# Kernel optimization log

Hardware: AMD Instinct MI355X
Metric: run time of the kernel (lower is better)

## Reference

```python
import jax, jax.numpy as jnp
import numpy as np

MIN_NORM = 1e-15


def _dist_matrix(offset, normal, c):
    # compute_rel (default path, trip_sel='all', abs/norm/hier_trip = False):
    # dist_matrix[i, j] = exp( dist2plane(x=offset[i], a=normal_scaled[j], p=offset[j], signed=True) )
    # normal_scaled = normal * (1 - c * ||offset||^2)  (conformal factor per row)
    conf = 1.0 - c * jnp.sum(offset * offset, axis=1, keepdims=True)  # [N,1]
    a = normal * conf                                                 # [N,d]
    x2 = jnp.sum(offset * offset, axis=1)                             # [N]
    gram = offset @ offset.T                                          # [N,N], <x_i, p_j>
    # mobius_add(-p_j, x_i, c): u = -p_j, v = x_i
    uv = -gram                                                        # <u_j, v_i>, indexed [i,j]
    coef_u = 1.0 + 2.0 * c * uv + c * x2[:, None]                     # multiplies u = -p_j
    coef_v = 1.0 - c * x2[None, :]                                    # multiplies v = x_i  (||u_j||^2 = x2[j])
    denom = 1.0 + 2.0 * c * uv + (c * c) * x2[None, :] * x2[:, None]
    denom = jnp.maximum(denom, MIN_NORM)
    # diff[i,j,:]  [N,N,d]
    diff = (coef_u[:, :, None] * (-offset)[None, :, :] + coef_v[:, :, None] * offset[:, None, :]) / denom[:, :, None]
    dn2 = jnp.maximum(jnp.sum(diff * diff, axis=-1), MIN_NORM)        # [N,N]
    sc_diff_a = jnp.einsum('ijd,jd->ij', diff, a)                     # signed inner product
    a_norm = jnp.maximum(jnp.linalg.norm(a, axis=-1), MIN_NORM)       # [N]
    sqrt_c = jnp.sqrt(c)
    num = 2.0 * sqrt_c * sc_diff_a
    den = jnp.maximum((1.0 - c * dn2) * a_norm[None, :], MIN_NORM)
    dist = jnp.arcsinh(num / den) / sqrt_c
    return jnp.exp(dist)  # default branch: dist_matrix = dist_matrix.exp()


def setup_inputs() -> dict:
    key = jax.random.key(0)
    k1, k2, k3 = jax.random.split(key, 3)
    N, d = 320, 256
    # points inside the Poincare ball (||offset|| ~ 0.5 < 1 for c = 1)
    offset = jax.random.normal(k1, (N, d), jnp.float32) * 0.03
    normal = jax.random.normal(k2, (N, d), jnp.float32)
    curv = jnp.ones((1,), jnp.float32)
    # sparse triplet validity mask, as produced by get_triplet_mask
    valid_indices = jax.random.bernoulli(k3, 0.01, (N, N, N))
    return {"offset": offset, "normal": normal, "curv": curv, "valid_indices": valid_indices}


def reference(offset, normal, curv, valid_indices):
    c = curv[0]
    margin = 0.0  # __init__ value; updated only in update_distance
    dm = _dist_matrix(offset, normal, c)                 # [N,N]
    # triplet_loss = margin - d(a,p) + d(a,n), masked, clamped at 0
    tl = margin - dm[:, :, None] + dm[:, None, :]        # [N,N,N]
    tl = valid_indices.astype(dm.dtype) * tl
    tl = jnp.maximum(tl, 0.0)
    # trip_sel == 'all': mean over entries > 1e-16
    pos = tl > 1e-16
    count = jnp.maximum(jnp.sum(pos), 1)
    loss = jnp.sum(jnp.where(pos, tl, 0.0)) / count
    return loss
```

## Files before the change

kernel.cpp:

```cpp
#include <hip/hip_runtime.h>
#include <math.h>

#define NPT 320
#define DDIM 256
#define NN2 (NPT*NPT)
#define MINN 1e-15f

#define CHUNKS 5
#define PLANE4 (NN2/4)
#define CHUNK4 (PLANE4/CHUNKS)
#define ITERS  (CHUNK4/256)
#define NBLK   (NPT*CHUNKS)

__global__ __launch_bounds__(256) void k_pre(const float* __restrict__ off,
                                             const float* __restrict__ nrm,
                                             const float* __restrict__ curv,
                                             float* __restrict__ dm) {
    __shared__ float sOI[16][260];
    __shared__ float sOJ[16][260];
    __shared__ float sNJ[16][260];
    __shared__ float sx2i[16], sx2j[16], snnj[16], spaj[16];
    const float c = curv[0];
    const float sqrtc = sqrtf(c);
    const int I0 = blockIdx.y * 16, J0 = blockIdx.x * 16;
    const int t = threadIdx.x;
    const int r = t >> 4;
    const int cc = t & 15;
    const int cb = cc << 4;

    const float4* pOI = (const float4*)&off[(I0 + r) * DDIM + cb];
    const float4* pOJ = (const float4*)&off[(J0 + r) * DDIM + cb];
    const float4* pNJ = (const float4*)&nrm[(J0 + r) * DDIM + cb];
#pragma unroll
    for (int q = 0; q < 4; ++q) {
        *(float4*)&sOI[r][cb + 4 * q] = pOI[q];
        *(float4*)&sOJ[r][cb + 4 * q] = pOJ[q];
        *(float4*)&sNJ[r][cb + 4 * q] = pNJ[q];
    }
    __syncthreads();

    float a0 = 0.f, a1 = 0.f, a2 = 0.f, a3 = 0.f;
#pragma unroll
    for (int q = 0; q < 16; ++q) {
        const float oi = sOI[r][cb + q];
        const float oj = sOJ[r][cb + q];
        const float nj = sNJ[r][cb + q];
        a0 = fmaf(oi, oi, a0);
        a1 = fmaf(oj, oj, a1);
        a2 = fmaf(nj, nj, a2);
        a3 = fmaf(oj, nj, a3);
    }
    for (int o = 1; o < 16; o <<= 1) {
        a0 += __shfl_xor(a0, o);
        a1 += __shfl_xor(a1, o);
        a2 += __shfl_xor(a2, o);
        a3 += __shfl_xor(a3, o);
    }
    if (cc == 0) { sx2i[r] = a0; sx2j[r] = a1; snnj[r] = a2; spaj[r] = a3; }
    __syncthreads();

    const int ti = t >> 4, tj = t & 15;
    float g = 0.f, h = 0.f;
#pragma unroll 8
    for (int d = 0; d < DDIM; ++d) {
        const float oi = sOI[ti][d];
        g = fmaf(oi, sOJ[tj][d], g);
        h = fmaf(oi, sNJ[tj][d], h);
    }

    const float x2i = sx2i[ti], x2j = sx2j[tj], nnj = snnj[tj], paj = spaj[tj];
    const float cu = 1.f - 2.f * c * g + c * x2i;
    const float cv = 1.f - c * x2j;
    float den0 = 1.f - 2.f * c * g + c * c * x2i * x2j;
    den0 = fmaxf(den0, MINN);
    float dn2 = (cu * cu * x2j - 2.f * cu * cv * g + cv * cv * x2i) / (den0 * den0);
    dn2 = fmaxf(dn2, MINN);
    const float sc = cv * (cv * h - cu * paj) / den0;
    const float an = fmaxf(fabsf(cv) * sqrtf(nnj), MINN);
    const float numv = 2.f * sqrtc * sc;
    const float denv = fmaxf((1.f - c * dn2) * an, MINN);
    const float z = numv / denv;
    const float dist = asinhf(z) / sqrtc;
    dm[(I0 + ti) * NPT + (J0 + tj)] = expf(dist);
}

__global__ __launch_bounds__(256) void k_trip(const int* __restrict__ mask,
                                              const float* __restrict__ dm,
                                              double* __restrict__ psum,
                                              unsigned* __restrict__ pcnt) {
    __shared__ __align__(16) float dmrow[NPT];
    const int bx = blockIdx.x;
    const int i = bx / CHUNKS;
    const int chunk = bx - i * CHUNKS;
    const int t = threadIdx.x;

    for (int v = t; v < NPT; v += 256) dmrow[v] = dm[i * NPT + v];
    __syncthreads();

    const int4* m4 = (const int4*)mask + (size_t)i * PLANE4 + (size_t)chunk * CHUNK4;
    const float4* dm4 = (const float4*)dmrow;

    float s = 0.f;
    unsigned cnt = 0;

#define PROC(B, U) { \
        const unsigned lin = (unsigned)(chunk * CHUNK4 + t + 256 * (U)); \
        const unsigned jj = lin / 80u; \
        const unsigned k4 = lin - jj * 80u; \
        const float dij = dmrow[jj]; \
        const float4 dk = dm4[k4]; \
        const float t0 = dk.x - dij, t1 = dk.y - dij, t2 = dk.z - dij, t3 = dk.w - dij; \
        const bool p0 = (B).x && (t0 > 1e-16f); \
        const bool p1 = (B).y && (t1 > 1e-16f); \
        const bool p2 = (B).z && (t2 > 1e-16f); \
        const bool p3 = (B).w && (t3 > 1e-16f); \
        s += p0 ? t0 : 0.f; cnt += p0; \
        s += p1 ? t1 : 0.f; cnt += p1; \
        s += p2 ? t2 : 0.f; cnt += p2; \
        s += p3 ? t3 : 0.f; cnt += p3; }

#pragma unroll 1
    for (int g = 0; g < ITERS / 4; ++g) {
        const int u0 = g * 4;
        const int4 b0 = m4[t + 256 * (u0 + 0)];
        const int4 b1 = m4[t + 256 * (u0 + 1)];
        const int4 b2 = m4[t + 256 * (u0 + 2)];
        const int4 b3 = m4[t + 256 * (u0 + 3)];
        PROC(b0, u0 + 0)
        PROC(b1, u0 + 1)
        PROC(b2, u0 + 2)
        PROC(b3, u0 + 3)
    }
#undef PROC

    double sd = (double)s;
    for (int o = 32; o; o >>= 1) {
        sd += __shfl_down(sd, o);
        cnt += __shfl_down(cnt, o);
    }
    __shared__ double ss[4];
    __shared__ unsigned scn[4];
    const int w = t >> 6;
    if ((t & 63) == 0) { ss[w] = sd; scn[w] = cnt; }
    __syncthreads();
    if (t == 0) {
        psum[bx] = ss[0] + ss[1] + ss[2] + ss[3];
        pcnt[bx] = scn[0] + scn[1] + scn[2] + scn[3];
    }
}

__global__ __launch_bounds__(256) void k_fin(const double* __restrict__ psum,
                                             const unsigned* __restrict__ pcnt,
                                             float* __restrict__ out) {
    const int t = threadIdx.x;
    double s = 0.0;
    unsigned long long c = 0ULL;
    for (int v = t; v < NBLK; v += 256) {
        s += psum[v];
        c += (unsigned long long)pcnt[v];
    }
    for (int o = 32; o; o >>= 1) {
        s += __shfl_down(s, o);
        c += __shfl_down(c, o);
    }
    __shared__ double ss[4];
    __shared__ unsigned long long sc[4];
    const int w = t >> 6;
    if ((t & 63) == 0) { ss[w] = s; sc[w] = c; }
    __syncthreads();
    if (t == 0) {
        const double S = ss[0] + ss[1] + ss[2] + ss[3];
        unsigned long long C = sc[0] + sc[1] + sc[2] + sc[3];
        if (C == 0ULL) C = 1ULL;
        out[0] = (float)(S / (double)C);
    }
}

extern "C" void kernel_launch(void* const* d_in, const int* in_sizes, int n_in,
                              void* d_out, int out_size, void* d_ws, size_t ws_size,
                              hipStream_t stream) {
    const float* off  = (const float*)d_in[0];
    const float* nrm  = (const float*)d_in[1];
    const float* curv = (const float*)d_in[2];
    const int*   mask = (const int*)d_in[3];
    float* out = (float*)d_out;

    char* ws = (char*)d_ws;
    float* dm = (float*)(ws + 64);
    double* psum = (double*)(ws + 64 + 409600);
    unsigned* pcnt = (unsigned*)(ws + 64 + 409600 + NBLK * 8);

    k_pre<<<dim3(NPT / 16, NPT / 16), 256, 0, stream>>>(off, nrm, curv, dm);
    k_trip<<<NBLK, 256, 0, stream>>>(mask, dm, psum, pcnt);
    k_fin<<<1, 256, 0, stream>>>(psum, pcnt, out);
}
```

Before: 37.97 us.

## Read k_pre operands from global memory and reshape k_trip grid to 320 threads

k_pre no longer stages the offset and normal rows in shared memory. Each thread now streams float4 rows directly from global memory for both the norm computation and the dot products, relying on cache reuse. k_trip switches to 8 chunks per row with 320 threads per block and fully unrolled mask loads (ten int4 loads per thread) to raise memory-level parallelism. The direct global loads in k_pre risk more cache traffic, since each row is reread many times without an explicit shared-memory copy.

```diff
diff --git a/kernel.cpp b/kernel.cpp
--- a/kernel.cpp
+++ b/kernel.cpp
@@ -6,19 +6,17 @@
 #define NN2 (NPT*NPT)
 #define MINN 1e-15f
 
-#define CHUNKS 5
+#define CHUNKS 8
 #define PLANE4 (NN2/4)
 #define CHUNK4 (PLANE4/CHUNKS)
-#define ITERS  (CHUNK4/256)
+#define TTHR   320
+#define ITERS  (CHUNK4/TTHR)
 #define NBLK   (NPT*CHUNKS)
 
 __global__ __launch_bounds__(256) void k_pre(const float* __restrict__ off,
                                              const float* __restrict__ nrm,
                                              const float* __restrict__ curv,
                                              float* __restrict__ dm) {
-    __shared__ float sOI[16][260];
-    __shared__ float sOJ[16][260];
-    __shared__ float sNJ[16][260];
     __shared__ float sx2i[16], sx2j[16], snnj[16], spaj[16];
     const float c = curv[0];
     const float sqrtc = sqrtf(c);
@@ -26,46 +24,46 @@
     const int t = threadIdx.x;
     const int r = t >> 4;
     const int cc = t & 15;
-    const int cb = cc << 4;
 
-    const float4* pOI = (const float4*)&off[(I0 + r) * DDIM + cb];
-    const float4* pOJ = (const float4*)&off[(J0 + r) * DDIM + cb];
-    const float4* pNJ = (const float4*)&nrm[(J0 + r) * DDIM + cb];
+    {
+        const float4* oi = (const float4*)&off[(I0 + r) * DDIM];
+        const float4* oj = (const float4*)&off[(J0 + r) * DDIM];
+        const float4* nj = (const float4*)&nrm[(J0 + r) * DDIM];
+        float a0 = 0.f, a1 = 0.f, a2 = 0.f, a3 = 0.f;
 #pragma unroll
-    for (int q = 0; q < 4; ++q) {
-        *(float4*)&sOI[r][cb + 4 * q] = pOI[q];
-        *(float4*)&sOJ[r][cb + 4 * q] = pOJ[q];
-        *(float4*)&sNJ[r][cb + 4 * q] = pNJ[q];
+        for (int q = 0; q < 4; ++q) {
+            const float4 x = oi[cc * 4 + q];
+            const float4 y = oj[cc * 4 + q];
+            const float4 z = nj[cc * 4 + q];
+            a0 = fmaf(x.x, x.x, fmaf(x.y, x.y, fmaf(x.z, x.z, fmaf(x.w, x.w, a0))));
+            a1 = fmaf(y.x, y.x, fmaf(y.y, y.y, fmaf(y.z, y.z, fmaf(y.w, y.w, a1))));
+            a2 = fmaf(z.x, z.x, fmaf(z.y, z.y, fmaf(z.z, z.z, fmaf(z.w, z.w, a2))));
+            a3 = fmaf(y.x, z.x, fmaf(y.y, z.y, fmaf(y.z, z.z, fmaf(y.w, z.w, a3))));
+        }
+        for (int o = 1; o < 16; o <<= 1) {
+            a0 += __shfl_xor(a0, o);
+            a1 += __shfl_xor(a1, o);
+            a2 += __shfl_xor(a2, o);
+            a3 += __shfl_xor(a3, o);
+        }
+        if (cc == 0) { sx2i[r] = a0; sx2j[r] = a1; snnj[r] = a2; spaj[r] = a3; }
     }
     __syncthreads();
 
-    float a0 = 0.f, a1 = 0.f, a2 = 0.f, a3 = 0.f;
-#pragma unroll
-    for (int q = 0; q < 16; ++q) {
-        const float oi = sOI[r][cb + q];
-        const float oj = sOJ[r][cb + q];
-        const float nj = sNJ[r][cb + q];
-        a0 = fmaf(oi, oi, a0);
-        a1 = fmaf(oj, oj, a1);
-        a2 = fmaf(nj, nj, a2);
-        a3 = fmaf(oj, nj, a3);
-    }
-    for (int o = 1; o < 16; o <<= 1) {
-        a0 += __shfl_xor(a0, o);
-        a1 += __shfl_xor(a1, o);
-        a2 += __shfl_xor(a2, o);
-        a3 += __shfl_xor(a3, o);
-    }
-    if (cc == 0) { sx2i[r] = a0; sx2j[r] = a1; snnj[r] = a2; spaj[r] = a3; }
-    __syncthreads();
-
-    const int ti = t >> 4, tj = t & 15;
+    const int ti = r, tj = cc;
+    const float4* rI = (const float4*)&off[(I0 + ti) * DDIM];
+    const float4* rJ = (const float4*)&off[(J0 + tj) * DDIM];
+    const float4* rN = (const float4*)&nrm[(J0 + tj) * DDIM];
     float g = 0.f, h = 0.f;
 #pragma unroll 8
-    for (int d = 0; d < DDIM; ++d) {
-        const float oi = sOI[ti][d];
-        g = fmaf(oi, sOJ[tj][d], g);
-        h = fmaf(oi, sNJ[tj][d], h);
+    for (int d4 = 0; d4 < DDIM / 4; ++d4) {
+        const float4 ai = rI[d4];
+        const float4 bj = rJ[d4];
+        const float4 nj = rN[d4];
+        g = fmaf(ai.x, bj.x, g); g = fmaf(ai.y, bj.y, g);
+        g = fmaf(ai.z, bj.z, g); g = fmaf(ai.w, bj.w, g);
+        h = fmaf(ai.x, nj.x, h); h = fmaf(ai.y, nj.y, h);
+        h = fmaf(ai.z, nj.z, h); h = fmaf(ai.w, nj.w, h);
     }
 
     const float x2i = sx2i[ti], x2j = sx2j[tj], nnj = snnj[tj], paj = spaj[tj];
@@ -84,27 +82,28 @@
     dm[(I0 + ti) * NPT + (J0 + tj)] = expf(dist);
 }
 
-__global__ __launch_bounds__(256) void k_trip(const int* __restrict__ mask,
-                                              const float* __restrict__ dm,
-                                              double* __restrict__ psum,
-                                              unsigned* __restrict__ pcnt) {
+__global__ __launch_bounds__(TTHR) void k_trip(const int* __restrict__ mask,
+                                               const float* __restrict__ dm,
+                                               double* __restrict__ psum,
+                                               unsigned* __restrict__ pcnt) {
     __shared__ __align__(16) float dmrow[NPT];
     const int bx = blockIdx.x;
-    const int i = bx / CHUNKS;
-    const int chunk = bx - i * CHUNKS;
+    const int i = bx >> 3;
+    const int chunk = bx & 7;
     const int t = threadIdx.x;
 
-    for (int v = t; v < NPT; v += 256) dmrow[v] = dm[i * NPT + v];
+    dmrow[t] = dm[i * NPT + t];
     __syncthreads();
 
     const int4* m4 = (const int4*)mask + (size_t)i * PLANE4 + (size_t)chunk * CHUNK4;
     const float4* dm4 = (const float4*)dmrow;
+    const unsigned lin0 = (unsigned)(chunk * CHUNK4 + t);
 
     float s = 0.f;
     unsigned cnt = 0;
 
 #define PROC(B, U) { \
-        const unsigned lin = (unsigned)(chunk * CHUNK4 + t + 256 * (U)); \
+        const unsigned lin = lin0 + TTHR * (U); \
         const unsigned jj = lin / 80u; \
         const unsigned k4 = lin - jj * 80u; \
         const float dij = dmrow[jj]; \
@@ -119,18 +118,14 @@
         s += p2 ? t2 : 0.f; cnt += p2; \
         s += p3 ? t3 : 0.f; cnt += p3; }
 
-#pragma unroll 1
-    for (int g = 0; g < ITERS / 4; ++g) {
-        const int u0 = g * 4;
-        const int4 b0 = m4[t + 256 * (u0 + 0)];
-        const int4 b1 = m4[t + 256 * (u0 + 1)];
-        const int4 b2 = m4[t + 256 * (u0 + 2)];
-        const int4 b3 = m4[t + 256 * (u0 + 3)];
-        PROC(b0, u0 + 0)
-        PROC(b1, u0 + 1)
-        PROC(b2, u0 + 2)
-        PROC(b3, u0 + 3)
-    }
+    int4 b0 = m4[t + TTHR * 0], b1 = m4[t + TTHR * 1];
+    int4 b2 = m4[t + TTHR * 2], b3 = m4[t + TTHR * 3];
+    int4 b4 = m4[t + TTHR * 4], b5 = m4[t + TTHR * 5];
+    int4 b6 = m4[t + TTHR * 6], b7 = m4[t + TTHR * 7];
+    PROC(b0, 0) PROC(b1, 1) PROC(b2, 2) PROC(b3, 3)
+    const int4 b8 = m4[t + TTHR * 8], b9 = m4[t + TTHR * 9];
+    PROC(b4, 4) PROC(b5, 5) PROC(b6, 6) PROC(b7, 7)
+    PROC(b8, 8) PROC(b9, 9)
 #undef PROC
 
     double sd = (double)s;
@@ -138,14 +133,14 @@
         sd += __shfl_down(sd, o);
         cnt += __shfl_down(cnt, o);
     }
-    __shared__ double ss[4];
-    __shared__ unsigned scn[4];
+    __shared__ double ss[5];
+    __shared__ unsigned scn[5];
     const int w = t >> 6;
     if ((t & 63) == 0) { ss[w] = sd; scn[w] = cnt; }
     __syncthreads();
     if (t == 0) {
-        psum[bx] = ss[0] + ss[1] + ss[2] + ss[3];
-        pcnt[bx] = scn[0] + scn[1] + scn[2] + scn[3];
+        psum[bx] = ss[0] + ss[1] + ss[2] + ss[3] + ss[4];
+        pcnt[bx] = scn[0] + scn[1] + scn[2] + scn[3] + scn[4];
     }
 }
 
@@ -191,6 +186,6 @@
     unsigned* pcnt = (unsigned*)(ws + 64 + 409600 + NBLK * 8);
 
     k_pre<<<dim3(NPT / 16, NPT / 16), 256, 0, stream>>>(off, nrm, curv, dm);
-    k_trip<<<NBLK, 256, 0, stream>>>(mask, dm, psum, pcnt);
+    k_trip<<<NBLK, TTHR, 0, stream>>>(mask, dm, psum, pcnt);
     k_fin<<<1, 256, 0, stream>>>(psum, pcnt, out);
 }
```

Result: slower. 65.13 us (+71.5%).
